# Kernel optimization log

Measured on AMD Instinct MI355X. Metric: run time of the kernel, lower is better.

The kernel has to match this reference:

```python
import jax, jax.numpy as jnp
import numpy as np

GAMMA = 0.25  # channel_gamma


def q_shift(x, h, w, gamma=GAMMA):
    # x: [B, T, C] with T == h*w; shift 4 channel groups by 1 pixel in 4 directions
    B, T, C = x.shape
    xi = x.reshape(B, h, w, C)
    c = int(C * gamma)
    g0 = jnp.pad(xi[:, :, :-1, 0:c],        ((0, 0), (0, 0), (1, 0), (0, 0)))  # right
    g1 = jnp.pad(xi[:, :, 1:, c:2 * c],     ((0, 0), (0, 0), (0, 1), (0, 0)))  # left
    g2 = jnp.pad(xi[:, :-1, :, 2 * c:3 * c], ((0, 0), (1, 0), (0, 0), (0, 0)))  # down
    g3 = jnp.pad(xi[:, 1:, :, 3 * c:4 * c],  ((0, 0), (0, 1), (0, 0), (0, 0)))  # up
    rest = xi[:, :, :, 4 * c:]
    return jnp.concatenate([g0, g1, g2, g3, rest], axis=-1).reshape(B, T, C)


def wkv(w_dec, u, k, v):
    # Numerically-stabilized RWKV WKV recurrence.
    # w_dec, u: [C]; k, v: [B, T, C] -> y: [B, T, C]
    B, T, C = k.shape
    kT = jnp.transpose(k, (1, 0, 2))  # [T, B, C]
    vT = jnp.transpose(v, (1, 0, 2))

    def step(carry, kv_t):
        p, q, o = carry  # running num/den and log-scale, each [B, C]
        kt, vt = kv_t
        no = jnp.maximum(o, u + kt)
        A = jnp.exp(o - no)
        Bf = jnp.exp(u + kt - no)
        y = (A * p + Bf * vt) / (A * q + Bf)
        no2 = jnp.maximum(w_dec + o, kt)
        A2 = jnp.exp(w_dec + o - no2)
        B2 = jnp.exp(kt - no2)
        return (A2 * p + B2 * vt, A2 * q + B2, no2), y

    init = (jnp.zeros((B, C), k.dtype), jnp.zeros((B, C), k.dtype),
            jnp.full((B, C), -1e38, k.dtype))
    _, yT = jax.lax.scan(step, init, (kT, vT))
    return jnp.transpose(yT, (1, 0, 2))


def layer_norm(x, g, b, eps=1e-5):
    mu = jnp.mean(x, axis=-1, keepdims=True)
    var = jnp.var(x, axis=-1, keepdims=True)
    return (x - mu) * jax.lax.rsqrt(var + eps) * g + b


def setup_inputs() -> dict:
    key = jax.random.key(0)
    ks = jax.random.split(key, 12)
    B, H, W, C = 16, 32, 32, 768
    T = H * W
    x = jax.random.normal(ks[0], (B, T, C), dtype=jnp.float32)
    return {
        "x": x,
        "h": H,
        "w": W,
        "spatial_decay": jax.random.normal(ks[1], (C,), jnp.float32) * 0.5,
        "spatial_first": jax.random.normal(ks[2], (C,), jnp.float32) * 0.5,
        "mix_k": jax.random.uniform(ks[3], (1, 1, C), jnp.float32),
        "mix_v": jax.random.uniform(ks[4], (1, 1, C), jnp.float32),
        "mix_r": jax.random.uniform(ks[5], (1, 1, C), jnp.float32),
        "W_k": jax.random.normal(ks[6], (C, C), jnp.float32) * 0.02,
        "W_v": jax.random.normal(ks[7], (C, C), jnp.float32) * 0.02,
        "W_r": jax.random.normal(ks[8], (C, C), jnp.float32) * 0.02,
        "W_o": jax.random.normal(ks[9], (C, C), jnp.float32) * 0.02,
        "ln_g": jnp.ones((C,), jnp.float32),
        "ln_b": jnp.zeros((C,), jnp.float32),
    }


def reference(x, h, w, spatial_decay, spatial_first, mix_k, mix_v, mix_r,
              W_k, W_v, W_r, W_o, ln_g, ln_b):
    B, T, C = x.shape
    xx = q_shift(x, h, w)
    xk = x * mix_k + xx * (1.0 - mix_k)
    xv = x * mix_v + xx * (1.0 - mix_v)
    xr = x * mix_r + xx * (1.0 - mix_r)
    k = xk @ W_k          # [B, T, C]
    v = xv @ W_v
    sr = jax.nn.sigmoid(xr @ W_r)
    y = wkv(spatial_decay / T, spatial_first / T, k, v)
    y = layer_norm(y, ln_g, ln_b)
    return (sr * y) @ W_o
```

## Files before the change

kernel.cpp:

```cpp
#include <hip/hip_runtime.h>
#include <hip/hip_bf16.h>

using bf16 = __hip_bfloat16;
typedef __attribute__((ext_vector_type(8))) __bf16 bf16x8;
typedef __attribute__((ext_vector_type(4))) float floatx4;

#define B_  16
#define T_  1024
#define C_  768
#define M_  16384

#define OFF_XK ((size_t)0)
#define OFF_XV ((size_t)25165824)
#define OFF_XR ((size_t)50331648)
#define OFF_K  ((size_t)75497472)
#define OFF_V  ((size_t)100663296)
#define OFF_SR ((size_t)125829120)
#define OFF_WT ((size_t)150994944)
#define OFF_Y  ((size_t)0)
#define OFF_Z  ((size_t)50331648)

struct __align__(16) BV8 { bf16 v[8]; };

__global__ __launch_bounds__(256) void transpose_w(
    const float* __restrict__ w0, const float* __restrict__ w1,
    const float* __restrict__ w2, const float* __restrict__ w3,
    bf16* __restrict__ wt) {
  __shared__ float tile[32][33];
  int which = blockIdx.z;
  const float* src = which == 0 ? w0 : which == 1 ? w1 : which == 2 ? w2 : w3;
  bf16* dst = wt + (size_t)which * (C_ * C_);
  int k0 = blockIdx.y * 32;
  int n0 = blockIdx.x * 32;
  int j  = threadIdx.x & 31;
  int i0 = threadIdx.x >> 5;
#pragma unroll
  for (int s = 0; s < 4; s++) {
    int i = i0 + s * 8;
    tile[i][j] = src[(size_t)(k0 + i) * C_ + n0 + j];
  }
  __syncthreads();
#pragma unroll
  for (int s = 0; s < 4; s++) {
    int i = i0 + s * 8;
    dst[(size_t)(n0 + i) * C_ + k0 + j] = __float2bfloat16(tile[j][i]);
  }
}

__global__ __launch_bounds__(256) void shift_mix(
    const float* __restrict__ x,
    const float* __restrict__ mk, const float* __restrict__ mv, const float* __restrict__ mr,
    bf16* __restrict__ xk, bf16* __restrict__ xv, bf16* __restrict__ xr) {
  int gid = blockIdx.x * 256 + threadIdx.x;
  int c8 = gid % 96;
  int bt = gid / 96;
  int b  = bt >> 10;
  int t  = bt & 1023;
  int hh = t >> 5, ww = t & 31;
  int c0 = c8 * 8;
  int g  = c8 / 24;
  int sh = hh, sw = ww;
  bool valid;
  if (g == 0)      { sw = ww - 1; valid = (ww >= 1);  }
  else if (g == 1) { sw = ww + 1; valid = (ww <= 30); }
  else if (g == 2) { sh = hh - 1; valid = (hh >= 1);  }
  else             { sh = hh + 1; valid = (hh <= 30); }
  size_t off = (size_t)bt * C_ + c0;
  float xs[8], ss[8];
  *(float4*)(xs)     = *(const float4*)(x + off);
  *(float4*)(xs + 4) = *(const float4*)(x + off + 4);
  if (valid) {
    size_t soff = (size_t)(b * 1024 + sh * 32 + sw) * C_ + c0;
    *(float4*)(ss)     = *(const float4*)(x + soff);
    *(float4*)(ss + 4) = *(const float4*)(x + soff + 4);
  } else {
#pragma unroll
    for (int j = 0; j < 8; j++) ss[j] = 0.f;
  }
  BV8 ok, ov, orr;
#pragma unroll
  for (int j = 0; j < 8; j++) {
    float xf = xs[j], sf = ss[j];
    float a  = mk[c0 + j];
    float bm = mv[c0 + j];
    float cm = mr[c0 + j];
    ok.v[j]  = __float2bfloat16(xf * a  + sf * (1.f - a));
    ov.v[j]  = __float2bfloat16(xf * bm + sf * (1.f - bm));
    orr.v[j] = __float2bfloat16(xf * cm + sf * (1.f - cm));
  }
  *(BV8*)(xk + off) = ok;
  *(BV8*)(xv + off) = ov;
  *(BV8*)(xr + off) = orr;
}

template <int MODE>
__global__ __launch_bounds__(256, 2) void gemm_bt(
    const bf16* __restrict__ A, const bf16* __restrict__ BT,
    void* __restrict__ Cout, int M, int N, int K) {
  __shared__ bf16 As[128 * 32];
  __shared__ bf16 Bs[128 * 32];
  int tid  = threadIdx.x;
  int wave = tid >> 6, lane = tid & 63;
  int wm = (wave & 1) * 64, wn = (wave >> 1) * 64;
  size_t m0 = (size_t)blockIdx.y * 128, n0 = (size_t)blockIdx.x * 128;

  floatx4 acc[4][4];
#pragma unroll
  for (int i = 0; i < 4; i++)
#pragma unroll
    for (int j = 0; j < 4; j++) acc[i][j] = (floatx4){0.f, 0.f, 0.f, 0.f};

  int row = tid >> 2;
  int kc  = (tid & 3) * 8;
  const bf16* Ab = A  + (m0 + row) * (size_t)K + kc;
  const bf16* Bb = BT + (n0 + row) * (size_t)K + kc;
  bf16* lA = As + tid * 8;
  bf16* lB = Bs + tid * 8;
  int fr  = lane & 15;
  int fko = (lane >> 4) * 8;

  for (int k0 = 0; k0 < K; k0 += 32) {
    __builtin_amdgcn_global_load_lds(
        (const __attribute__((address_space(1))) void*)(Ab + k0),
        (__attribute__((address_space(3))) void*)lA, 16, 0, 0);
    __builtin_amdgcn_global_load_lds(
        (const __attribute__((address_space(1))) void*)(Ab + (size_t)64 * K + k0),
        (__attribute__((address_space(3))) void*)(lA + 2048), 16, 0, 0);
    __builtin_amdgcn_global_load_lds(
        (const __attribute__((address_space(1))) void*)(Bb + k0),
        (__attribute__((address_space(3))) void*)lB, 16, 0, 0);
    __builtin_amdgcn_global_load_lds(
        (const __attribute__((address_space(1))) void*)(Bb + (size_t)64 * K + k0),
        (__attribute__((address_space(3))) void*)(lB + 2048), 16, 0, 0);
    __syncthreads();
    bf16x8 af[4], bfr[4];
#pragma unroll
    for (int mi = 0; mi < 4; mi++)
      af[mi] = *(const bf16x8*)(As + (wm + mi * 16 + fr) * 32 + fko);
#pragma unroll
    for (int ni = 0; ni < 4; ni++)
      bfr[ni] = *(const bf16x8*)(Bs + (wn + ni * 16 + fr) * 32 + fko);
#pragma unroll
    for (int mi = 0; mi < 4; mi++)
#pragma unroll
      for (int ni = 0; ni < 4; ni++)
        acc[mi][ni] = __builtin_amdgcn_mfma_f32_16x16x32_bf16(
            af[mi], bfr[ni], acc[mi][ni], 0, 0, 0);
    __syncthreads();
  }
  int cr = (lane >> 4) * 4;
  int cc = lane & 15;
#pragma unroll
  for (int mi = 0; mi < 4; mi++)
#pragma unroll
    for (int ni = 0; ni < 4; ni++)
#pragma unroll
      for (int i = 0; i < 4; i++) {
        size_t r   = m0 + wm + mi * 16 + cr + i;
        size_t col = n0 + wn + ni * 16 + cc;
        float val = acc[mi][ni][i];
        if (MODE == 3) {
          ((float*)Cout)[r * N + col] = val;
        } else {
          if (MODE == 2) val = 1.0f / (1.0f + __expf(-val));
          ((bf16*)Cout)[r * N + col] = __float2bfloat16(val);
        }
      }
}

#define SEG 32
#define SL  32
__global__ __launch_bounds__(256) void wkv_chunked(
    const bf16* __restrict__ kT, const bf16* __restrict__ vT,
    const float* __restrict__ sd, const float* __restrict__ sf,
    float* __restrict__ y) {
  int tid = threadIdx.x;
  int s = tid >> 3, cr = tid & 7;
  int b = blockIdx.x / 96, cg = blockIdx.x % 96;
  int c = cg * 8 + cr;
  float w = sd[c] * (1.0f / (float)T_);
  float u = sf[c] * (1.0f / (float)T_);
  size_t base = (size_t)c * M_ + b * T_ + s * SL;
  BV8 kv[4], vv8[4];
#pragma unroll
  for (int j = 0; j < 4; j++) {
    kv[j]  = *(const BV8*)(kT + base + j * 8);
    vv8[j] = *(const BV8*)(vT + base + j * 8);
  }
  float P = 0.f, Q = 0.f, O = -1e38f;
#pragma unroll
  for (int j = 0; j < 4; j++)
#pragma unroll
    for (int i = 0; i < 8; i++) {
      float kt = __bfloat162float(kv[j].v[i]);
      float vt = __bfloat162float(vv8[j].v[i]);
      float wo = w + O;
      float no = fmaxf(wo, kt);
      float A  = __expf(wo - no);
      float Bx = __expf(kt - no);
      P = A * P + Bx * vt;
      Q = A * Q + Bx;
      O = no;
    }
  __shared__ float sP[SEG][8], sQ[SEG][8], sO[SEG][8];
  sP[s][cr] = P; sQ[s][cr] = Q; sO[s][cr] = O;
  __syncthreads();
  if (s == 0) {
    float p = 0.f, q = 0.f, o = -1e38f;
    float dw = (float)SL * w;
#pragma unroll 1
    for (int t = 0; t < SEG; t++) {
      float Pp = sP[t][cr], Qq = sQ[t][cr], Oo = sO[t][cr];
      sP[t][cr] = p; sQ[t][cr] = q; sO[t][cr] = o;
      float a  = dw + o;
      float no = fmaxf(a, Oo);
      float e1 = __expf(a - no);
      float e2 = __expf(Oo - no);
      p = e1 * p + e2 * Pp;
      q = e1 * q + e2 * Qq;
      o = no;
    }
  }
  __syncthreads();
  float p = sP[s][cr], q = sQ[s][cr], o = sO[s][cr];
  float* yp = y + ((size_t)(b * T_ + s * SL)) * C_ + c;
#pragma unroll
  for (int j = 0; j < 4; j++)
#pragma unroll
    for (int i = 0; i < 8; i++) {
      float kt = __bfloat162float(kv[j].v[i]);
      float vt = __bfloat162float(vv8[j].v[i]);
      float uk = u + kt;
      float no = fmaxf(o, uk);
      float A  = __expf(o - no);
      float Bx = __expf(uk - no);
      yp[(size_t)(j * 8 + i) * C_] = __fdividef(A * p + Bx * vt, A * q + Bx);
      float wo  = w + o;
      float no2 = fmaxf(wo, kt);
      float A2 = __expf(wo - no2);
      float B2 = __expf(kt - no2);
      p = A2 * p + B2 * vt;
      q = A2 * q + B2;
      o = no2;
    }
}

__global__ __launch_bounds__(256) void ln_sr_kernel(
    const float* __restrict__ y, const bf16* __restrict__ sr,
    const float* __restrict__ gg, const float* __restrict__ bb,
    bf16* __restrict__ z) {
  int rowi = blockIdx.x;
  size_t base = (size_t)rowi * C_;
  int tid = threadIdx.x;
  float v0 = y[base + tid], v1 = y[base + tid + 256], v2 = y[base + tid + 512];
  float s  = v0 + v1 + v2;
  float s2 = v0 * v0 + v1 * v1 + v2 * v2;
#pragma unroll
  for (int off = 32; off > 0; off >>= 1) {
    s  += __shfl_down(s, off);
    s2 += __shfl_down(s2, off);
  }
  __shared__ float red[16];
  int wv = tid >> 6, ln = tid & 63;
  if (ln == 0) { red[wv] = s; red[8 + wv] = s2; }
  __syncthreads();
  if (tid == 0) {
    float ts = red[0] + red[1] + red[2] + red[3];
    float t2 = red[8] + red[9] + red[10] + red[11];
    float mu  = ts * (1.0f / (float)C_);
    float var = t2 * (1.0f / (float)C_) - mu * mu;
    red[0] = mu;
    red[1] = rsqrtf(var + 1e-5f);
  }
  __syncthreads();
  float mu = red[0], rs = red[1];
#pragma unroll
  for (int j = 0; j < 3; j++) {
    int c = tid + j * 256;
    float val = (j == 0 ? v0 : (j == 1 ? v1 : v2));
    float gn  = gg[c];
    float bn  = bb[c];
    float srf = __bfloat162float(sr[base + c]);
    z[base + c] = __float2bfloat16(((val - mu) * rs * gn + bn) * srf);
  }
}

extern "C" void kernel_launch(void* const* d_in, const int* in_sizes, int n_in,
                              void* d_out, int out_size, void* d_ws, size_t ws_size,
                              hipStream_t stream) {
  const float* x  = (const float*)d_in[0];
  const float* sd = (const float*)d_in[3];
  const float* sf = (const float*)d_in[4];
  const float* mk = (const float*)d_in[5];
  const float* mv = (const float*)d_in[6];
  const float* mr = (const float*)d_in[7];
  const float* Wk = (const float*)d_in[8];
  const float* Wv = (const float*)d_in[9];
  const float* Wr = (const float*)d_in[10];
  const float* Wo = (const float*)d_in[11];
  const float* lg = (const float*)d_in[12];
  const float* lb = (const float*)d_in[13];

  char* ws = (char*)d_ws;
  bf16* xk  = (bf16*)(ws + OFF_XK);
  bf16* xv  = (bf16*)(ws + OFF_XV);
  bf16* xr  = (bf16*)(ws + OFF_XR);
  bf16* kTb = (bf16*)(ws + OFF_K);
  bf16* vTb = (bf16*)(ws + OFF_V);
  bf16* srb = (bf16*)(ws + OFF_SR);
  bf16* wt  = (bf16*)(ws + OFF_WT);
  bf16* WkT = wt;
  bf16* WvT = wt + (size_t)C_ * C_;
  bf16* WrT = wt + (size_t)2 * C_ * C_;
  bf16* WoT = wt + (size_t)3 * C_ * C_;
  float* yb = (float*)(ws + OFF_Y);
  bf16*  zb = (bf16*)(ws + OFF_Z);

  transpose_w<<<dim3(24, 24, 4), 256, 0, stream>>>(Wk, Wv, Wr, Wo, wt);
  shift_mix<<<(M_ * 96) / 256, 256, 0, stream>>>(x, mk, mv, mr, xk, xv, xr);

  dim3 tgrid(M_ / 128, C_ / 128);
  gemm_bt<1><<<tgrid, 256, 0, stream>>>(WkT, xk, kTb, C_, M_, C_);
  gemm_bt<1><<<tgrid, 256, 0, stream>>>(WvT, xv, vTb, C_, M_, C_);
  dim3 ggrid(C_ / 128, M_ / 128);
  gemm_bt<2><<<ggrid, 256, 0, stream>>>(xr, WrT, srb, M_, C_, C_);

  wkv_chunked<<<B_ * 96, 256, 0, stream>>>(kTb, vTb, sd, sf, yb);
  ln_sr_kernel<<<M_, 256, 0, stream>>>(yb, srb, lg, lb, zb);

  gemm_bt<3><<<ggrid, 256, 0, stream>>>(zb, WoT, (float*)d_out, M_, C_, C_);
}
```

Measured before the change: 313.5 us.

## Double GEMM K-tile, merge K/V GEMMs into one launch, store WKV output as bf16

The GEMM body now stages a 64-wide K slice per iteration, split into two 32-wide sub-tiles in LDS, which halves the number of barriers per tile at the cost of doubled LDS use. The K and V projection GEMMs are combined into one launch through a z grid dimension, so the two GEMMs share a grid. The WKV output is written as bf16 instead of fp32, halving the traffic into the layernorm kernel, with some loss of precision before normalization.

Result: faster. 305.7 us (-2.5%).

```diff
diff --git a/kernel.cpp b/kernel.cpp
--- a/kernel.cpp
+++ b/kernel.cpp
@@ -94,15 +94,16 @@
 }
 
 template <int MODE>
-__global__ __launch_bounds__(256, 2) void gemm_bt(
+__device__ __forceinline__ void gemm_body(
     const bf16* __restrict__ A, const bf16* __restrict__ BT,
-    void* __restrict__ Cout, int M, int N, int K) {
-  __shared__ bf16 As[128 * 32];
-  __shared__ bf16 Bs[128 * 32];
+    void* __restrict__ Cout, int M, int N, int K,
+    int bx, int by) {
+  __shared__ bf16 As[128 * 64];
+  __shared__ bf16 Bs[128 * 64];
   int tid  = threadIdx.x;
   int wave = tid >> 6, lane = tid & 63;
   int wm = (wave & 1) * 64, wn = (wave >> 1) * 64;
-  size_t m0 = (size_t)blockIdx.y * 128, n0 = (size_t)blockIdx.x * 128;
+  size_t m0 = (size_t)by * 128, n0 = (size_t)bx * 128;
 
   floatx4 acc[4][4];
 #pragma unroll
@@ -110,42 +111,44 @@
 #pragma unroll
     for (int j = 0; j < 4; j++) acc[i][j] = (floatx4){0.f, 0.f, 0.f, 0.f};
 
-  int row = tid >> 2;
-  int kc  = (tid & 3) * 8;
-  const bf16* Ab = A  + (m0 + row) * (size_t)K + kc;
-  const bf16* Bb = BT + (n0 + row) * (size_t)K + kc;
+  int srow[4], skk[4];
+#pragma unroll
+  for (int i = 0; i < 4; i++) {
+    srow[i] = ((tid >> 2) + i * 64) & 127;
+    skk[i]  = (tid & 3) * 8 + (i >> 1) * 32;
+  }
   bf16* lA = As + tid * 8;
   bf16* lB = Bs + tid * 8;
   int fr  = lane & 15;
   int fko = (lane >> 4) * 8;
 
-  for (int k0 = 0; k0 < K; k0 += 32) {
-    __builtin_amdgcn_global_load_lds(
-        (const __attribute__((address_space(1))) void*)(Ab + k0),
-        (__attribute__((address_space(3))) void*)lA, 16, 0, 0);
-    __builtin_amdgcn_global_load_lds(
-        (const __attribute__((address_space(1))) void*)(Ab + (size_t)64 * K + k0),
-        (__attribute__((address_space(3))) void*)(lA + 2048), 16, 0, 0);
-    __builtin_amdgcn_global_load_lds(
-        (const __attribute__((address_space(1))) void*)(Bb + k0),
-        (__attribute__((address_space(3))) void*)lB, 16, 0, 0);
-    __builtin_amdgcn_global_load_lds(
-        (const __attribute__((address_space(1))) void*)(Bb + (size_t)64 * K + k0),
-        (__attribute__((address_space(3))) void*)(lB + 2048), 16, 0, 0);
+  for (int k0 = 0; k0 < K; k0 += 64) {
+#pragma unroll
+    for (int i = 0; i < 4; i++) {
+      __builtin_amdgcn_global_load_lds(
+          (const __attribute__((address_space(1))) void*)(A + (m0 + srow[i]) * (size_t)K + k0 + skk[i]),
+          (__attribute__((address_space(3))) void*)(lA + i * 2048), 16, 0, 0);
+      __builtin_amdgcn_global_load_lds(
+          (const __attribute__((address_space(1))) void*)(BT + (n0 + srow[i]) * (size_t)K + k0 + skk[i]),
+          (__attribute__((address_space(3))) void*)(lB + i * 2048), 16, 0, 0);
+    }
     __syncthreads();
-    bf16x8 af[4], bfr[4];
-#pragma unroll
-    for (int mi = 0; mi < 4; mi++)
-      af[mi] = *(const bf16x8*)(As + (wm + mi * 16 + fr) * 32 + fko);
-#pragma unroll
-    for (int ni = 0; ni < 4; ni++)
-      bfr[ni] = *(const bf16x8*)(Bs + (wn + ni * 16 + fr) * 32 + fko);
-#pragma unroll
-    for (int mi = 0; mi < 4; mi++)
+#pragma unroll
+    for (int s = 0; s < 2; s++) {
+      bf16x8 af[4], bfr[4];
+#pragma unroll
+      for (int mi = 0; mi < 4; mi++)
+        af[mi] = *(const bf16x8*)(As + s * 4096 + (wm + mi * 16 + fr) * 32 + fko);
 #pragma unroll
       for (int ni = 0; ni < 4; ni++)
-        acc[mi][ni] = __builtin_amdgcn_mfma_f32_16x16x32_bf16(
-            af[mi], bfr[ni], acc[mi][ni], 0, 0, 0);
+        bfr[ni] = *(const bf16x8*)(Bs + s * 4096 + (wn + ni * 16 + fr) * 32 + fko);
+#pragma unroll
+      for (int mi = 0; mi < 4; mi++)
+#pragma unroll
+        for (int ni = 0; ni < 4; ni++)
+          acc[mi][ni] = __builtin_amdgcn_mfma_f32_16x16x32_bf16(
+              af[mi], bfr[ni], acc[mi][ni], 0, 0, 0);
+    }
     __syncthreads();
   }
   int cr = (lane >> 4) * 4;
@@ -168,12 +171,29 @@
       }
 }
 
+template <int MODE>
+__global__ __launch_bounds__(256, 2) void gemm_bt(
+    const bf16* __restrict__ A, const bf16* __restrict__ BT,
+    void* __restrict__ Cout, int M, int N, int K) {
+  gemm_body<MODE>(A, BT, Cout, M, N, K, blockIdx.x, blockIdx.y);
+}
+
+__global__ __launch_bounds__(256, 2) void gemm_kv(
+    const bf16* __restrict__ A0, const bf16* __restrict__ B0, bf16* __restrict__ C0,
+    const bf16* __restrict__ A1, const bf16* __restrict__ B1, bf16* __restrict__ C1,
+    int M, int N, int K) {
+  if (blockIdx.z == 0)
+    gemm_body<1>(A0, B0, C0, M, N, K, blockIdx.x, blockIdx.y);
+  else
+    gemm_body<1>(A1, B1, C1, M, N, K, blockIdx.x, blockIdx.y);
+}
+
 #define SEG 32
 #define SL  32
 __global__ __launch_bounds__(256) void wkv_chunked(
     const bf16* __restrict__ kT, const bf16* __restrict__ vT,
     const float* __restrict__ sd, const float* __restrict__ sf,
-    float* __restrict__ y) {
+    bf16* __restrict__ y) {
   int tid = threadIdx.x;
   int s = tid >> 3, cr = tid & 7;
   int b = blockIdx.x / 96, cg = blockIdx.x % 96;
@@ -223,7 +243,7 @@
   }
   __syncthreads();
   float p = sP[s][cr], q = sQ[s][cr], o = sO[s][cr];
-  float* yp = y + ((size_t)(b * T_ + s * SL)) * C_ + c;
+  bf16* yp = y + ((size_t)(b * T_ + s * SL)) * C_ + c;
 #pragma unroll
   for (int j = 0; j < 4; j++)
 #pragma unroll
@@ -234,7 +254,8 @@
       float no = fmaxf(o, uk);
       float A  = __expf(o - no);
       float Bx = __expf(uk - no);
-      yp[(size_t)(j * 8 + i) * C_] = __fdividef(A * p + Bx * vt, A * q + Bx);
+      yp[(size_t)(j * 8 + i) * C_] =
+          __float2bfloat16(__fdividef(A * p + Bx * vt, A * q + Bx));
       float wo  = w + o;
       float no2 = fmaxf(wo, kt);
       float A2 = __expf(wo - no2);
@@ -246,13 +267,15 @@
 }
 
 __global__ __launch_bounds__(256) void ln_sr_kernel(
-    const float* __restrict__ y, const bf16* __restrict__ sr,
+    const bf16* __restrict__ y, const bf16* __restrict__ sr,
     const float* __restrict__ gg, const float* __restrict__ bb,
     bf16* __restrict__ z) {
   int rowi = blockIdx.x;
   size_t base = (size_t)rowi * C_;
   int tid = threadIdx.x;
-  float v0 = y[base + tid], v1 = y[base + tid + 256], v2 = y[base + tid + 512];
+  float v0 = __bfloat162float(y[base + tid]);
+  float v1 = __bfloat162float(y[base + tid + 256]);
+  float v2 = __bfloat162float(y[base + tid + 512]);
   float s  = v0 + v1 + v2;
   float s2 = v0 * v0 + v1 * v1 + v2 * v2;
 #pragma unroll
@@ -313,15 +336,14 @@
   bf16* WvT = wt + (size_t)C_ * C_;
   bf16* WrT = wt + (size_t)2 * C_ * C_;
   bf16* WoT = wt + (size_t)3 * C_ * C_;
-  float* yb = (float*)(ws + OFF_Y);
-  bf16*  zb = (bf16*)(ws + OFF_Z);
+  bf16* yb  = (bf16*)(ws + OFF_Y);
+  bf16* zb  = (bf16*)(ws + OFF_Z);
 
   transpose_w<<<dim3(24, 24, 4), 256, 0, stream>>>(Wk, Wv, Wr, Wo, wt);
   shift_mix<<<(M_ * 96) / 256, 256, 0, stream>>>(x, mk, mv, mr, xk, xv, xr);
 
-  dim3 tgrid(M_ / 128, C_ / 128);
-  gemm_bt<1><<<tgrid, 256, 0, stream>>>(WkT, xk, kTb, C_, M_, C_);
-  gemm_bt<1><<<tgrid, 256, 0, stream>>>(WvT, xv, vTb, C_, M_, C_);
+  gemm_kv<<<dim3(M_ / 128, C_ / 128, 2), 256, 0, stream>>>(
+      WkT, xk, kTb, WvT, xv, vTb, C_, M_, C_);
   dim3 ggrid(C_ / 128, M_ / 128);
   gemm_bt<2><<<ggrid, 256, 0, stream>>>(xr, WrT, srb, M_, C_, C_);
 
```
